# Performance work log

Measured on AMD Instinct MI355X. Metric: run time of the kernel, lower is better.

Reference implementation:

```python
import jax, jax.numpy as jnp
import numpy as np

B, N, E, D, NS, H = 32, 4096, 256, 256, 8, 256
N_ITERS, N_SH, N_MESH, MESH_LR = 3, 5, 4, 5.0

def layer_norm(x, scale, bias, eps=1e-5):
    m = jnp.mean(x, axis=-1, keepdims=True)
    v = jnp.var(x, axis=-1, keepdims=True)
    return (x - m) / jnp.sqrt(v + eps) * scale + bias

def sinkhorn(C, a, b, u=None, v=None, n_iters=N_SH):
    # log-domain Sinkhorn with marginals a [B,N], b [B,S]; C [B,N,S]
    log_a, log_b = jnp.log(a), jnp.log(b)
    if u is None:
        u = jnp.zeros_like(a)
    if v is None:
        v = jnp.zeros_like(b)
    K = -C
    for _ in range(n_iters):
        u = log_a - jax.nn.logsumexp(K + v[:, None, :], axis=-1)
        v = log_b - jax.nn.logsumexp(K + u[:, :, None], axis=-2)
    attn = jnp.exp(K + u[:, :, None] + v[:, None, :])
    return attn, u, v

def minimize_entropy_of_sinkhorn(C0, a, b, mesh_lr=MESH_LR, n_mesh=N_MESH):
    # MESH: gradient-descend the cost matrix to minimize entropy of the transport plan
    def ent(C):
        attn, _, _ = sinkhorn(C, a, b)
        return -jnp.sum(attn * jnp.log(attn + 1e-8))
    C = C0
    for _ in range(n_mesh):
        C = C - mesh_lr * jax.grad(ent)(C)
    _, u, v = sinkhorn(C, a, b)
    return C, u, v

def gru_cell(x, h, Wih, Whh, bih, bhh):
    # torch.nn.GRUCell math, gate order (r, z, n)
    gi = x @ Wih.T + bih
    gh = h @ Whh.T + bhh
    ir, iz, inn = jnp.split(gi, 3, axis=-1)
    hr, hz, hn = jnp.split(gh, 3, axis=-1)
    r = jax.nn.sigmoid(ir + hr)
    z = jax.nn.sigmoid(iz + hz)
    n = jnp.tanh(inn + r * hn)
    return (1.0 - z) * n + z * h

def setup_inputs():
    key = jax.random.key(0)
    ks = jax.random.split(key, 16)
    s = 0.02
    return {
        "inputs": jax.random.normal(ks[0], (B, N, E), jnp.float32),
        "slots_init": jax.random.normal(ks[1], (B, NS, D), jnp.float32),
        "ln_in_s": jnp.ones((E,), jnp.float32), "ln_in_b": jnp.zeros((E,), jnp.float32),
        "ln_sl_s": jnp.ones((D,), jnp.float32), "ln_sl_b": jnp.zeros((D,), jnp.float32),
        "ln_mlp_s": jnp.ones((D,), jnp.float32), "ln_mlp_b": jnp.zeros((D,), jnp.float32),
        "Wq": jax.random.normal(ks[2], (D, D), jnp.float32) * s,
        "Wk": jax.random.normal(ks[3], (E, D), jnp.float32) * s,
        "Wv": jax.random.normal(ks[4], (E, D), jnp.float32) * s,
        "wi_W": jax.random.normal(ks[5], (E, 1), jnp.float32) * s, "wi_b": jnp.zeros((1,), jnp.float32),
        "ws_W": jax.random.normal(ks[6], (D, 1), jnp.float32) * s, "ws_b": jnp.zeros((1,), jnp.float32),
        "gru_Wih": jax.random.normal(ks[7], (3 * D, D), jnp.float32) * s,
        "gru_Whh": jax.random.normal(ks[8], (3 * D, D), jnp.float32) * s,
        "gru_bih": jnp.zeros((3 * D,), jnp.float32), "gru_bhh": jnp.zeros((3 * D,), jnp.float32),
        "mlp_W1": jax.random.normal(ks[9], (D, H), jnp.float32) * s, "mlp_b1": jnp.zeros((H,), jnp.float32),
        "mlp_W2": jax.random.normal(ks[10], (H, D), jnp.float32) * s, "mlp_b2": jnp.zeros((D,), jnp.float32),
    }

def reference(inputs, slots_init, ln_in_s, ln_in_b, ln_sl_s, ln_sl_b, ln_mlp_s, ln_mlp_b, Wq, Wk, Wv, wi_W, wi_b, ws_W, ws_b, gru_Wih, gru_Whh, gru_bih, gru_bhh, mlp_W1, mlp_b1, mlp_W2, mlp_b2):
    x = layer_norm(inputs, ln_in_s, ln_in_b)
    k = x @ Wk          # [B,N,D]
    v = x @ Wv          # [B,N,D]
    a = jax.nn.softmax(jnp.squeeze(x @ wi_W, -1) + wi_b[0], axis=-1) * NS  # input marginal [B,N]
    k_sq = jnp.sum(k * k, axis=-1)  # [B,N]

    def step(slots):
        sn = layer_norm(slots, ln_sl_s, ln_sl_b)
        b = jax.nn.softmax(jnp.squeeze(sn @ ws_W, -1) + ws_b[0], axis=-1) * NS  # slot marginal [B,S]
        q = sn @ Wq  # [B,S,D]
        # Euclidean cdist(k, q) via the Gram-matrix identity
        d2 = k_sq[:, :, None] + jnp.sum(q * q, -1)[:, None, :] - 2.0 * jnp.einsum('bnd,bsd->bns', k, q)
        C = jnp.sqrt(jnp.clip(d2, 1e-12))
        C, p, qpot = minimize_entropy_of_sinkhorn(C, a, b)
        attn, _, _ = sinkhorn(C, a, b, u=p, v=qpot)  # warm-started final sinkhorn
        updates = jnp.einsum('bns,bnd->bsd', attn, v)
        h = gru_cell(updates.reshape(-1, D), slots.reshape(-1, D), gru_Wih, gru_Whh, gru_bih, gru_bhh).reshape(B, NS, D)
        hn = layer_norm(h, ln_mlp_s, ln_mlp_b)
        h = h + (jax.nn.relu(hn @ mlp_W1 + mlp_b1) @ mlp_W2 + mlp_b2)
        return h, attn

    slots = slots_init
    attn = None
    for _ in range(N_ITERS - 1):
        slots, attn = step(slots)
    slots = jax.lax.stop_gradient(slots)  # .detach() before final step
    slots, attn = step(slots)
    return slots, jnp.transpose(attn, (0, 2, 1)), slots
```

## Files before the change

kernel.cpp:

```cpp
#include <hip/hip_runtime.h>
#include <hip/hip_bf16.h>

#define B_ 32
#define N_ 4096
#define E_ 256
#define D_ 256
#define NS_ 8
#define LN8 2.0794415416798357f
#define OFF_ATTN 65536
#define OFF_S2   (65536 + 1048576)
#define NSPLIT 8
#define SENT 0xFFFFFFFFu

typedef unsigned short u16;
typedef unsigned short u16x8 __attribute__((ext_vector_type(8)));
typedef __bf16 bf16x8 __attribute__((ext_vector_type(8)));
typedef float floatx4 __attribute__((ext_vector_type(4)));

__device__ __forceinline__ float bf2f(u16 h) {
  unsigned int u = ((unsigned int)h) << 16;
  return __uint_as_float(u);
}
__device__ __forceinline__ u16 f2bf(float f) {
  unsigned int u = __float_as_uint(f);
  unsigned int r = (u + 0x7FFFu + ((u >> 16) & 1u)) >> 16;
  return (u16)r;
}
__device__ __forceinline__ float ldx(const void* p, int i, int dt) {
  return dt ? ((const float*)p)[i] : bf2f(((const u16*)p)[i]);
}
__device__ __forceinline__ void stx(void* p, size_t i, int dt, float v) {
  if (dt) ((float*)p)[i] = v; else ((u16*)p)[i] = f2bf(v);
}
__device__ __forceinline__ float slog(float x) { return __logf(fmaxf(x, 1e-35f)); }
__device__ __forceinline__ float cl(float x) { return fminf(fmaxf(x, -1e30f), 1e30f); }

__device__ __forceinline__ float breduce256(float v, float* red4, int tid) {
  #pragma unroll
  for (int m = 1; m < 64; m <<= 1) v += __shfl_xor(v, m, 64);
  __syncthreads();
  if ((tid & 63) == 0) red4[tid >> 6] = v;
  __syncthreads();
  return red4[0] + red4[1] + red4[2] + red4[3];
}

__global__ void detect_dtype_kernel(const u16* __restrict__ inp, int* __restrict__ flag) {
  int lane = threadIdx.x & 63;
  int good = 0;
  for (int i = lane; i < 256; i += 64) {
    float x = bf2f(inp[i]);
    float ax = fabsf(x);
    if (x == 0.0f || (ax >= 1e-3f && ax <= 64.0f)) good++;
  }
  #pragma unroll
  for (int m = 1; m < 64; m <<= 1) good += __shfl_xor(good, m, 64);
  if (lane == 0) *flag = (good >= 208) ? 0 : 1;
}


__global__ void transpose_any_kernel(const void* __restrict__ src, u16* __restrict__ dst,
                                     int R, int C, const int* __restrict__ dtf) {
  const int dt = *dtf;
  int idx = blockIdx.x * 256 + threadIdx.x;
  if (idx >= R * C) return;
  int r = idx / C, c = idx - r * C;
  dst[c * R + r] = f2bf(ldx(src, idx, dt));
}

__global__ void cast_slots_kernel(const void* __restrict__ src, float* __restrict__ dst,
                                  const int* __restrict__ dtf) {
  const int dt = *dtf;
  int i = blockIdx.x * 256 + threadIdx.x;
  dst[i] = ldx(src, i, dt);
}

__global__ __launch_bounds__(256) void ln_stats_kernel(
    const void* __restrict__ inp, const void* __restrict__ lns, const void* __restrict__ lnb,
    const void* __restrict__ wiW, const int* __restrict__ dtf,
    u16* __restrict__ xln, float* __restrict__ logits) {
  const int dt = *dtf;
  int row = blockIdx.x * 4 + (threadIdx.x >> 6);
  int lane = threadIdx.x & 63;
  float xs[4];
  if (dt) {
    float4 h = *(const float4*)((const float*)inp + (size_t)row * E_ + lane * 4);
    xs[0] = h.x; xs[1] = h.y; xs[2] = h.z; xs[3] = h.w;
  } else {
    ushort4 h = *(const ushort4*)((const u16*)inp + (size_t)row * E_ + lane * 4);
    xs[0] = bf2f(h.x); xs[1] = bf2f(h.y); xs[2] = bf2f(h.z); xs[3] = bf2f(h.w);
  }
  float s = xs[0] + xs[1] + xs[2] + xs[3];
  float q = xs[0]*xs[0] + xs[1]*xs[1] + xs[2]*xs[2] + xs[3]*xs[3];
  #pragma unroll
  for (int m = 1; m < 64; m <<= 1) { s += __shfl_xor(s, m, 64); q += __shfl_xor(q, m, 64); }
  float mean = s * (1.0f / E_);
  float var = q * (1.0f / E_) - mean * mean;
  float rstd = rsqrtf(fmaxf(var, 0.0f) + 1e-5f);
  int e = lane * 4;
  float d = 0.0f;
  float xn[4];
  #pragma unroll
  for (int j = 0; j < 4; ++j) {
    xn[j] = (xs[j] - mean) * rstd * ldx(lns, e + j, dt) + ldx(lnb, e + j, dt);
    d += xn[j] * ldx(wiW, e + j, dt);
  }
  ushort4 o;
  o.x = f2bf(xn[0]); o.y = f2bf(xn[1]); o.z = f2bf(xn[2]); o.w = f2bf(xn[3]);
  *(ushort4*)(xln + (size_t)row * E_ + e) = o;
  #pragma unroll
  for (int m = 1; m < 64; m <<= 1) d += __shfl_xor(d, m, 64);
  if (lane == 0) logits[row] = d;
}

__global__ __launch_bounds__(1024) void amarg_kernel(const float* __restrict__ logits,
    float* __restrict__ log_a, float* __restrict__ inva) {
  __shared__ float red[16];
  __shared__ float bcast;
  int b = blockIdx.x, tid = threadIdx.x;
  logits += (size_t)b * N_;
  float l[4];
  #pragma unroll
  for (int i = 0; i < 4; ++i) l[i] = logits[tid + i * 1024];
  float mx = fmaxf(fmaxf(l[0], l[1]), fmaxf(l[2], l[3]));
  #pragma unroll
  for (int m = 1; m < 64; m <<= 1) mx = fmaxf(mx, __shfl_xor(mx, m, 64));
  __syncthreads();
  if ((tid & 63) == 0) red[tid >> 6] = mx;
  __syncthreads();
  if (tid == 0) { float v = red[0]; for (int i = 1; i < 16; ++i) v = fmaxf(v, red[i]); bcast = v; }
  __syncthreads();
  float M = bcast;
  float se = 0.0f;
  #pragma unroll
  for (int i = 0; i < 4; ++i) se += __expf(l[i] - M);
  #pragma unroll
  for (int m = 1; m < 64; m <<= 1) se += __shfl_xor(se, m, 64);
  __syncthreads();
  if ((tid & 63) == 0) red[tid >> 6] = se;
  __syncthreads();
  if (tid == 0) { float v = 0; for (int i = 0; i < 16; ++i) v += red[i]; bcast = v; }
  __syncthreads();
  float lgS = slog(bcast);
  #pragma unroll
  for (int i = 0; i < 4; ++i) {
    float lav = l[i] - M - lgS + LN8;
    log_a[tid + i * 1024] = lav;
    inva[tid + i * 1024] = fminf(__expf(-lav), 1e20f);
  }
}

__global__ __launch_bounds__(256, 2) void gemm_bt_kernel(
    const u16* __restrict__ A, const u16* __restrict__ BT, u16* __restrict__ out) {
  __shared__ __align__(16) u16 Als[128 * 32];
  __shared__ __align__(16) u16 Bls[128 * 32];
  int tid = threadIdx.x;
  int m0 = blockIdx.x * 128, n0 = blockIdx.y * 128;
  int w = tid >> 6, lane = tid & 63;
  int wm = (w & 1) * 64, wn = (w >> 1) * 64;
  int fr = lane & 15, kg = lane >> 4;
  floatx4 acc[4][4];
  #pragma unroll
  for (int i = 0; i < 4; ++i)
    #pragma unroll
    for (int j = 0; j < 4; ++j) acc[i][j] = (floatx4){0.f, 0.f, 0.f, 0.f};
  int sm = tid >> 1;
  int sk0 = (tid & 1) * 16;
  const u16* arow = A + (size_t)(m0 + sm) * E_;
  const u16* brow = BT + (size_t)(n0 + sm) * E_;
  for (int kc = 0; kc < E_; kc += 32) {
    #pragma unroll
    for (int j = 0; j < 16; j += 8) {
      int kk = kc + sk0 + j;
      *(u16x8*)&Als[sm * 32 + sk0 + j] = *(const u16x8*)(arow + kk);
      *(u16x8*)&Bls[sm * 32 + sk0 + j] = *(const u16x8*)(brow + kk);
    }
    __syncthreads();
    bf16x8 af[4], bfv[4];
    #pragma unroll
    for (int im = 0; im < 4; ++im) af[im] = *(const bf16x8*)&Als[(wm + im * 16 + fr) * 32 + kg * 8];
    #pragma unroll
    for (int in = 0; in < 4; ++in) bfv[in] = *(const bf16x8*)&Bls[(wn + in * 16 + fr) * 32 + kg * 8];
    #pragma unroll
    for (int im = 0; im < 4; ++im)
      #pragma unroll
      for (int in = 0; in < 4; ++in)
        acc[im][in] = __builtin_amdgcn_mfma_f32_16x16x32_bf16(af[im], bfv[in], acc[im][in], 0, 0, 0);
    __syncthreads();
  }
  #pragma unroll
  for (int im = 0; im < 4; ++im)
    #pragma unroll
    for (int in = 0; in < 4; ++in)
      #pragma unroll
      for (int r = 0; r < 4; ++r) {
        int row = m0 + wm + im * 16 + kg * 4 + r;
        int col = n0 + wn + in * 16 + fr;
        out[(size_t)row * D_ + col] = f2bf(acc[im][in][r]);
      }
}


__global__ __launch_bounds__(256) void s1_kernel(
    const float* __restrict__ slots, const void* __restrict__ lnss, const void* __restrict__ lnsb,
    const void* __restrict__ Wq, const void* __restrict__ wsW, const int* __restrict__ dtf,
    float* __restrict__ qf, float* __restrict__ q_sq, float* __restrict__ logits_b) {
  __shared__ float sn_sh[256];
  __shared__ float red4[4];
  const int dt = *dtf;
  int row = blockIdx.x;
  int tid = threadIdx.x;
  float h = slots[(size_t)row * D_ + tid];
  float sum = breduce256(h, red4, tid);
  float sq = breduce256(h * h, red4, tid);
  float mean = sum * (1.0f / D_), var = sq * (1.0f / D_) - mean * mean;
  float rstd = rsqrtf(fmaxf(var, 0.0f) + 1e-5f);
  float sn = (h - mean) * rstd * ldx(lnss, tid, dt) + ldx(lnsb, tid, dt);
  sn_sh[tid] = sn;
  __syncthreads();
  float acc = 0.0f;
  if (dt) {
    const float* W = (const float*)Wq;
    for (int d = 0; d < 256; ++d) acc += sn_sh[d] * W[d * 256 + tid];
  } else {
    const u16* W = (const u16*)Wq;
    for (int d = 0; d < 256; ++d) acc += sn_sh[d] * bf2f(W[d * 256 + tid]);
  }
  qf[(size_t)row * 256 + tid] = acc;
  float qs = breduce256(acc * acc, red4, tid);
  float lbp = breduce256(sn * ldx(wsW, tid, dt), red4, tid);
  if (tid == 0) { q_sq[row] = qs; logits_b[row] = lbp; }
}

__global__ void bmarg_kernel(const float* __restrict__ logits_b, const void* __restrict__ wsb,
                             const int* __restrict__ dtf, float* __restrict__ log_b) {
  int b = threadIdx.x;
  if (b >= 32) return;
  float off = ldx(wsb, 0, *dtf);
  float l[8], M = -1e30f;
  #pragma unroll
  for (int s = 0; s < 8; ++s) { l[s] = logits_b[b * 8 + s] + off; M = fmaxf(M, l[s]); }
  float S = 0.0f;
  #pragma unroll
  for (int s = 0; s < 8; ++s) S += __expf(l[s] - M);
  float lgS = slog(S);
  #pragma unroll
  for (int s = 0; s < 8; ++s) log_b[b * 8 + s] = l[s] - M - lgS + LN8;
}

__device__ __forceinline__ float grp_sync_reduce(
    float acc8[8], float (*red)[8],
    unsigned int* gp, int rp, int blkn, int wv, int lane, int tid) {
  #pragma unroll
  for (int m = 1; m < 64; m <<= 1)
    #pragma unroll
    for (int s = 0; s < 8; ++s) acc8[s] += __shfl_xor(acc8[s], m, 64);
  if (lane == 0)
    #pragma unroll
    for (int s = 0; s < 8; ++s) red[wv][s] = acc8[s];
  __syncthreads();
  float x = 0.0f;
  if (tid < 64) {
    float v = red[tid >> 3][tid & 7];
    v += __shfl_xor(v, 8, 64);
    v += __shfl_xor(v, 16, 64);
    v += __shfl_xor(v, 32, 64);
    if (tid < 8)
      __hip_atomic_store(gp + rp * 64 + blkn * 8 + tid, __float_as_uint(v),
                         __ATOMIC_RELAXED, __HIP_MEMORY_SCOPE_AGENT);
    unsigned int u;
    for (;;) {
      u = __hip_atomic_load(gp + rp * 64 + tid, __ATOMIC_RELAXED, __HIP_MEMORY_SCOPE_AGENT);
      if (__all(u != SENT)) break;
      __builtin_amdgcn_s_sleep(1);
    }
    x = __uint_as_float(u);
    x += __shfl_xor(x, 8, 64);
    x += __shfl_xor(x, 16, 64);
    x += __shfl_xor(x, 32, 64);
  }
  return x;
}

__global__ __launch_bounds__(512, 2) void mesh_kernel(
    const u16* __restrict__ kbf, const u16* __restrict__ vbf,
    const float* __restrict__ qf32, const float* __restrict__ qsq_g,
    const float* __restrict__ log_a_g, const float* __restrict__ inva_g,
    const float* __restrict__ log_b_g, const int* __restrict__ dtf,
    unsigned int* __restrict__ gpart,
    float* __restrict__ updp, void* __restrict__ dout_or_null) {
  const int blkn = blockIdx.x;
  const int b = blockIdx.y;
  const int tid = threadIdx.x;
  const int dt = *dtf;
  const int n = blkn * 512 + tid;

  __shared__ float evP[6][8];
  __shared__ float lb[8], invb[8];
  __shared__ float dv[8];
  __shared__ float red[8][8];
  __shared__ float q_lds[8][256];
  __shared__ float qsq_l[8];
  __shared__ float pv_lds[512][8];

  const float la = log_a_g[(size_t)b * N_ + n];
  const float ia = inva_g[(size_t)b * N_ + n];
  unsigned int* gp = gpart + (size_t)b * 64 * 64;

  {
    const float* qb = qf32 + (size_t)b * 8 * 256;
    #pragma unroll
    for (int i = tid; i < 2048; i += 512) q_lds[i >> 8][i & 255] = qb[i];
    if (tid < 8) {
      qsq_l[tid] = qsq_g[b * 8 + tid];
      float x = log_b_g[b * 8 + tid];
      lb[tid] = x; invb[tid] = fminf(__expf(-x), 1e20f);
    }
  }
  __syncthreads();

  float E[8], dK[8], eus[5];
  float eu = 0.0f, dup = 0.0f;
  {
    const u16* kp = kbf + ((size_t)b * N_ + n) * D_;
    float accq[8] = {0, 0, 0, 0, 0, 0, 0, 0};
    float kq = 0.0f;
    for (int kc = 0; kc < 256; kc += 8) {
      u16x8 kv = *(const u16x8*)(kp + kc);
      float kf[8];
      #pragma unroll
      for (int j = 0; j < 8; ++j) { kf[j] = bf2f(kv[j]); kq += kf[j] * kf[j]; }
      #pragma unroll
      for (int s = 0; s < 8; ++s) {
        float4 qa = *(const float4*)&q_lds[s][kc];
        float4 qb2 = *(const float4*)&q_lds[s][kc + 4];
        accq[s] += kf[0] * qa.x + kf[1] * qa.y + kf[2] * qa.z + kf[3] * qa.w
                 + kf[4] * qb2.x + kf[5] * qb2.y + kf[6] * qb2.z + kf[7] * qb2.w;
      }
    }
    #pragma unroll
    for (int s = 0; s < 8; ++s) {
      float d2 = kq + qsq_l[s] - 2.0f * accq[s];
      float Cv = sqrtf(fmaxf(d2, 1e-12f));
      E[s] = __expf(-Cv);
    }
  }

  const int wv = tid >> 6, lane = tid & 63;
  int rp = 0;

  for (int mesh = 0; mesh < 4; ++mesh) {
    if (tid < 8) evP[0][tid] = 1.0f;
    __syncthreads();
    for (int t = 1; t <= 5; ++t) {
      float evp[8];
      #pragma unroll
      for (int s = 0; s < 8; ++s) evp[s] = evP[t - 1][s];
      float su = 0.0f;
      #pragma unroll
      for (int s = 0; s < 8; ++s) su += fminf(E[s] * evp[s], 1e30f);
      float u = la - slog(su);
      eu = fminf(__expf(u), 1e20f);
      eus[t - 1] = eu;
      float acc8[8];
      #pragma unroll
      for (int s = 0; s < 8; ++s) acc8[s] = fminf(E[s] * eu, 1e30f);
      float S = grp_sync_reduce(acc8, red, gp, rp, blkn, wv, lane, tid);
      if (tid < 8) {
        float v = lb[tid] - slog(S);
        evP[t][tid] = fminf(__expf(v), 1e20f);
      }
      ++rp;
      __syncthreads();
    }
    {
      float ev5[8];
      #pragma unroll
      for (int s = 0; s < 8; ++s) ev5[s] = evP[5][s];
      float acc8[8];
      dup = 0.0f;
      #pragma unroll
      for (int s = 0; s < 8; ++s) {
        float t1 = fminf(E[s] * eu, 1e30f);
        float P = fminf(t1 * ev5[s], 1e30f);
        float Pe = P + 1e-8f;
        float g = -(__logf(Pe) + P / Pe) * P;
        dK[s] = g; dup += g; acc8[s] = g;
      }
      float S = grp_sync_reduce(acc8, red, gp, rp, blkn, wv, lane, tid);
      if (tid < 8) dv[tid] = cl(S);
      ++rp;
      __syncthreads();
    }
    for (int t = 5; t >= 1; --t) {
      float evt[8], evtm[8], dvl[8], ibl[8];
      #pragma unroll
      for (int s = 0; s < 8; ++s) { evt[s] = evP[t][s]; evtm[s] = evP[t - 1][s]; dvl[s] = dv[s]; ibl[s] = invb[s]; }
      float eut = eus[t - 1];
      float duv = 0.0f;
      float w8[8];
      #pragma unroll
      for (int s = 0; s < 8; ++s) {
        float a1 = fminf(E[s] * eut, 1e30f);
        float b1 = fminf(a1 * evt[s], 1e30f);
        w8[s] = fminf(b1 * ibl[s], 1e30f);
        duv += cl(dvl[s] * w8[s]);
      }
      float du = ((t == 5) ? dup : 0.0f) - duv;
      float duf = cl(cl(du * ia) * eut);
      float acc8[8];
      #pragma unroll
      for (int s = 0; s < 8; ++s) {
        float ee = fminf(E[s] * evtm[s], 1e30f);
        float zc = cl(ee * duf);
        dK[s] -= cl(dvl[s] * w8[s]) + zc;
        acc8[s] = -zc;
      }
      if (t > 1) {
        float S = grp_sync_reduce(acc8, red, gp, rp, blkn, wv, lane, tid);
        if (tid < 8) dv[tid] = cl(S);
        ++rp;
      }
      __syncthreads();
    }
    #pragma unroll
    for (int s = 0; s < 8; ++s) {
      float dkc = fminf(fmaxf(dK[s], -4.0f), 4.0f);
      float Enew = E[s] * __expf(-5.0f * dkc);
      E[s] = fminf(fmaxf(Enew, 1e-35f), 1e30f);
    }
  }

  if (tid < 8) evP[0][tid] = 1.0f;
  __syncthreads();
  for (int t = 1; t <= 10; ++t) {
    int pc = (t - 1) & 1, cc = t & 1;
    float evp[8];
    #pragma unroll
    for (int s = 0; s < 8; ++s) evp[s] = evP[pc][s];
    float su = 0.0f;
    #pragma unroll
    for (int s = 0; s < 8; ++s) su += fminf(E[s] * evp[s], 1e30f);
    eu = fminf(__expf(la - slog(su)), 1e20f);
    float acc8[8];
    #pragma unroll
    for (int s = 0; s < 8; ++s) acc8[s] = fminf(E[s] * eu, 1e30f);
    float S = grp_sync_reduce(acc8, red, gp, rp, blkn, wv, lane, tid);
    if (tid < 8) {
      float v = lb[tid] - slog(S);
      evP[cc][tid] = fminf(__expf(v), 1e20f);
    }
    ++rp;
    __syncthreads();
  }
  float evf[8];
  #pragma unroll
  for (int s = 0; s < 8; ++s) evf[s] = evP[0][s];
  float pv[8];
  #pragma unroll
  for (int s = 0; s < 8; ++s) {
    float t1 = fminf(E[s] * eu, 1e30f);
    pv[s] = fminf(t1 * evf[s], 1e30f);
  }
  if (dout_or_null) {
    #pragma unroll
    for (int s = 0; s < 8; ++s)
      stx(dout_or_null, (size_t)OFF_ATTN + ((size_t)b * 8 + s) * N_ + n, dt, pv[s]);
  }

  #pragma unroll
  for (int s = 0; s < 8; ++s) pv_lds[tid][s] = pv[s];
  __syncthreads();
  {
    int d = tid & 255, half = tid >> 8;
    const u16* vp = vbf + ((size_t)b * N_ + blkn * 512 + half * 256) * D_ + d;
    float acc[8] = {0, 0, 0, 0, 0, 0, 0, 0};
    for (int i = 0; i < 256; ++i) {
      float vv = bf2f(vp[(size_t)i * D_]);
      float4 a0 = *(const float4*)&pv_lds[half * 256 + i][0];
      float4 a1 = *(const float4*)&pv_lds[half * 256 + i][4];
      acc[0] += a0.x * vv; acc[1] += a0.y * vv; acc[2] += a0.z * vv; acc[3] += a0.w * vv;
      acc[4] += a1.x * vv; acc[5] += a1.y * vv; acc[6] += a1.z * vv; acc[7] += a1.w * vv;
    }
    __syncthreads();
    if (half == 1) {
      #pragma unroll
      for (int s = 0; s < 8; ++s) pv_lds[d][s] = acc[s];
    }
    __syncthreads();
    if (half == 0) {
      #pragma unroll
      for (int s = 0; s < 8; ++s) acc[s] += pv_lds[d][s];
      #pragma unroll
      for (int s = 0; s < 8; ++s)
        updp[(((size_t)b * 8 + blkn) * 8 + s) * D_ + d] = acc[s];
    }
  }
}

__global__ __launch_bounds__(256) void gru_mlp_kernel(
    const float* __restrict__ updp, const float* __restrict__ slots_cur,
    const u16* __restrict__ WihT, const u16* __restrict__ WhhT,
    const void* __restrict__ bih, const void* __restrict__ bhh,
    const void* __restrict__ lnms, const void* __restrict__ lnmb,
    const void* __restrict__ W1, const void* __restrict__ b1,
    const void* __restrict__ W2, const void* __restrict__ b2,
    const int* __restrict__ dtf,
    float* __restrict__ slots_next, void* __restrict__ dout_or_null) {
  __shared__ float xs[256], hs[256], hns[256], as_[256];
  __shared__ float red4[4];
  const int dt = *dtf;
  int row = blockIdx.x;
  int b = row >> 3, s = row & 7;
  int tid = threadIdx.x;
  float x = 0.0f;
  #pragma unroll
  for (int c = 0; c < 8; ++c) x += updp[(((size_t)b * 8 + c) * 8 + s) * D_ + tid];
  float h = slots_cur[(size_t)row * D_ + tid];
  xs[tid] = x; hs[tid] = h;
  __syncthreads();
  float gr = ldx(bih, tid, dt), gz = ldx(bih, 256 + tid, dt), gn = ldx(bih, 512 + tid, dt);
  float hr = ldx(bhh, tid, dt), hz = ldx(bhh, 256 + tid, dt), hn_ = ldx(bhh, 512 + tid, dt);
  for (int e = 0; e < 256; ++e) {
    float xe = xs[e], he = hs[e];
    const u16* wi = WihT + e * 768;
    const u16* wh = WhhT + e * 768;
    gr += xe * bf2f(wi[tid]); gz += xe * bf2f(wi[256 + tid]); gn += xe * bf2f(wi[512 + tid]);
    hr += he * bf2f(wh[tid]); hz += he * bf2f(wh[256 + tid]); hn_ += he * bf2f(wh[512 + tid]);
  }
  float r = 1.0f / (1.0f + __expf(-(gr + hr)));
  float z = 1.0f / (1.0f + __expf(-(gz + hz)));
  float nn = tanhf(gn + r * hn_);
  float h2 = (1.0f - z) * nn + z * h;
  float sum = breduce256(h2, red4, tid);
  float sq = breduce256(h2 * h2, red4, tid);
  float mean = sum * (1.0f / D_), var = sq * (1.0f / D_) - mean * mean;
  float rstd = rsqrtf(fmaxf(var, 0.0f) + 1e-5f);
  float hn2 = (h2 - mean) * rstd * ldx(lnms, tid, dt) + ldx(lnmb, tid, dt);
  hns[tid] = hn2;
  __syncthreads();
  float a1 = ldx(b1, tid, dt);
  if (dt) {
    const float* W = (const float*)W1;
    for (int e = 0; e < 256; ++e) a1 += hns[e] * W[e * 256 + tid];
  } else {
    const u16* W = (const u16*)W1;
    for (int e = 0; e < 256; ++e) a1 += hns[e] * bf2f(W[e * 256 + tid]);
  }
  a1 = fmaxf(a1, 0.0f);
  as_[tid] = a1;
  __syncthreads();
  float o = h2 + ldx(b2, tid, dt);
  if (dt) {
    const float* W = (const float*)W2;
    for (int e = 0; e < 256; ++e) o += as_[e] * W[e * 256 + tid];
  } else {
    const u16* W = (const u16*)W2;
    for (int e = 0; e < 256; ++e) o += as_[e] * bf2f(W[e * 256 + tid]);
  }
  slots_next[(size_t)row * D_ + tid] = o;
  if (dout_or_null) {
    stx(dout_or_null, (size_t)row * D_ + tid, dt, o);
    stx(dout_or_null, (size_t)OFF_S2 + (size_t)row * D_ + tid, dt, o);
  }
}


extern "C" void kernel_launch(void* const* d_in, const int* in_sizes, int n_in,
                              void* d_out, int out_size, void* d_ws, size_t ws_size,
                              hipStream_t stream) {
  (void)in_sizes; (void)n_in; (void)out_size;
  const void* inp      = d_in[0];
  const void* slots0   = d_in[1];
  const void* ln_in_s  = d_in[2];
  const void* ln_in_b  = d_in[3];
  const void* ln_sl_s  = d_in[4];
  const void* ln_sl_b  = d_in[5];
  const void* ln_mlp_s = d_in[6];
  const void* ln_mlp_b = d_in[7];
  const void* Wq  = d_in[8];
  const void* Wk  = d_in[9];
  const void* Wv  = d_in[10];
  const void* wiW = d_in[11];
  const void* wsW = d_in[13];
  const void* wsb = d_in[14];
  const void* Wih = d_in[15];
  const void* Whh = d_in[16];
  const void* bih = d_in[17];
  const void* bhh = d_in[18];
  const void* W1  = d_in[19];
  const void* b1  = d_in[20];
  const void* W2  = d_in[21];
  const void* b2  = d_in[22];

  char* ws = (char*)d_ws;
  size_t off = 0;
  auto alloc = [&](size_t bytes) -> void* {
    void* p = ws + off;
    off += (bytes + 255) & ~(size_t)255;
    return p;
  };
  const size_t NR = (size_t)B_ * N_;
  int* dtflag     = (int*)alloc(256);
  float* logits_a = (float*)alloc(NR * 4);
  float* log_a    = (float*)alloc(NR * 4);
  float* inva     = (float*)alloc(NR * 4);
  u16* xln        = (u16*)alloc(NR * E_ * 2);
  u16* kbf        = (u16*)alloc(NR * D_ * 2);
  u16* vbf        = (u16*)alloc(NR * D_ * 2);
  u16* WkT        = (u16*)alloc(E_ * D_ * 2);
  u16* WvT        = (u16*)alloc(E_ * D_ * 2);
  u16* WihT       = (u16*)alloc(768 * 256 * 2);
  u16* WhhT       = (u16*)alloc(768 * 256 * 2);
  float* qf32     = (float*)alloc((size_t)B_ * 8 * 256 * 4);
  float* q_sq     = (float*)alloc(B_ * 8 * 4);
  float* logits_b = (float*)alloc(B_ * 8 * 4);
  float* log_b    = (float*)alloc(B_ * 8 * 4);
  float* updp     = (float*)alloc((size_t)B_ * 8 * 8 * D_ * 4);
  float* slots_a  = (float*)alloc((size_t)B_ * 8 * D_ * 4);
  float* slots_b  = (float*)alloc((size_t)B_ * 8 * D_ * 4);
  unsigned int* gpart = (unsigned int*)alloc((size_t)3 * B_ * 64 * 64 * 4);
  if (ws_size < off) return;

  hipMemsetAsync(gpart, 0xFF, (size_t)3 * B_ * 64 * 64 * 4, stream);
  detect_dtype_kernel<<<1, 64, 0, stream>>>((const u16*)inp, dtflag);

  transpose_any_kernel<<<(E_ * D_ + 255) / 256, 256, 0, stream>>>(Wk, WkT, E_, D_, dtflag);
  transpose_any_kernel<<<(E_ * D_ + 255) / 256, 256, 0, stream>>>(Wv, WvT, E_, D_, dtflag);
  transpose_any_kernel<<<(768 * 256 + 255) / 256, 256, 0, stream>>>(Wih, WihT, 768, 256, dtflag);
  transpose_any_kernel<<<(768 * 256 + 255) / 256, 256, 0, stream>>>(Whh, WhhT, 768, 256, dtflag);
  cast_slots_kernel<<<(B_ * 8 * D_) / 256, 256, 0, stream>>>(slots0, slots_a, dtflag);
  ln_stats_kernel<<<NR / 4, 256, 0, stream>>>(inp, ln_in_s, ln_in_b, wiW, dtflag, xln, logits_a);
  amarg_kernel<<<B_, 1024, 0, stream>>>(logits_a, log_a, inva);
  gemm_bt_kernel<<<dim3(NR / 128, 2), 256, 0, stream>>>(xln, WkT, kbf);
  gemm_bt_kernel<<<dim3(NR / 128, 2), 256, 0, stream>>>(xln, WvT, vbf);

  float* scur = slots_a;
  float* snext = slots_b;
  for (int step = 0; step < 3; ++step) {
    bool last = (step == 2);
    s1_kernel<<<B_ * 8, 256, 0, stream>>>(scur, ln_sl_s, ln_sl_b, Wq, wsW, dtflag, qf32, q_sq, logits_b);
    bmarg_kernel<<<1, 32, 0, stream>>>(logits_b, wsb, dtflag, log_b);
    mesh_kernel<<<dim3(NSPLIT, B_), 512, 0, stream>>>(kbf, vbf, qf32, q_sq, log_a, inva, log_b,
                                                      dtflag, gpart + (size_t)step * B_ * 64 * 64,
                                                      updp, last ? d_out : (void*)nullptr);
    gru_mlp_kernel<<<B_ * 8, 256, 0, stream>>>(updp, scur, WihT, WhhT, bih, bhh,
                                               ln_mlp_s, ln_mlp_b, W1, b1, W2, b2, dtflag, snext,
                                               last ? d_out : (void*)nullptr);
    float* t = scur; scur = snext; snext = t;
  }
}
```

Measured before the change: 1.028 ms.

## Fuse small kernels to cut launch count across setup and slot loop

Merges the four weight transposes into two kernels and the K and V projections into a single GEMM launch over a concatenated transposed weight. The slot-marginal softmax moves inside the mesh kernel, and the next step's slot layernorm/query projection is folded into the tail of the GRU/MLP kernel. The aim is to remove per-launch overhead and the serial gaps between tiny kernels. In exchange, the mesh kernel does some redundant per-block softmax work and the GRU kernel gets longer with extra block reductions.

```diff
diff --git a/kernel.cpp b/kernel.cpp
--- a/kernel.cpp
+++ b/kernel.cpp
@@ -58,13 +58,26 @@
 }
 
 
-__global__ void transpose_any_kernel(const void* __restrict__ src, u16* __restrict__ dst,
-                                     int R, int C, const int* __restrict__ dtf) {
+__global__ void tr_kv_kernel(const void* __restrict__ Wk, const void* __restrict__ Wv,
+                             u16* __restrict__ WkvT, const int* __restrict__ dtf) {
   const int dt = *dtf;
   int idx = blockIdx.x * 256 + threadIdx.x;
-  if (idx >= R * C) return;
-  int r = idx / C, c = idx - r * C;
-  dst[c * R + r] = f2bf(ldx(src, idx, dt));
+  int half = idx >> 16, i = idx & 65535;
+  int r = i >> 8, c = i & 255;
+  const void* src = half ? Wv : Wk;
+  WkvT[((size_t)(half * 256 + c)) * 256 + r] = f2bf(ldx(src, i, dt));
+}
+
+__global__ void tr_gru_kernel(const void* __restrict__ Wih, const void* __restrict__ Whh,
+                              u16* __restrict__ WihT, u16* __restrict__ WhhT,
+                              const int* __restrict__ dtf) {
+  const int dt = *dtf;
+  int idx = blockIdx.x * 256 + threadIdx.x;
+  int half = idx >= 196608;
+  int i = idx - (half ? 196608 : 0);
+  int r = i >> 8, c = i & 255;
+  u16* dst = half ? WhhT : WihT;
+  dst[(size_t)c * 768 + r] = f2bf(ldx(half ? Whh : Wih, i, dt));
 }
 
 __global__ void cast_slots_kernel(const void* __restrict__ src, float* __restrict__ dst,
@@ -150,11 +163,14 @@
 }
 
 __global__ __launch_bounds__(256, 2) void gemm_bt_kernel(
-    const u16* __restrict__ A, const u16* __restrict__ BT, u16* __restrict__ out) {
+    const u16* __restrict__ A, const u16* __restrict__ BT,
+    u16* __restrict__ kbf, u16* __restrict__ vbf) {
   __shared__ __align__(16) u16 Als[128 * 32];
   __shared__ __align__(16) u16 Bls[128 * 32];
   int tid = threadIdx.x;
   int m0 = blockIdx.x * 128, n0 = blockIdx.y * 128;
+  u16* ob = (n0 < 256) ? kbf : vbf;
+  int nb = n0 & 255;
   int w = tid >> 6, lane = tid & 63;
   int wm = (w & 1) * 64, wn = (w >> 1) * 64;
   int fr = lane & 15, kg = lane >> 4;
@@ -194,8 +210,8 @@
       #pragma unroll
       for (int r = 0; r < 4; ++r) {
         int row = m0 + wm + im * 16 + kg * 4 + r;
-        int col = n0 + wn + in * 16 + fr;
-        out[(size_t)row * D_ + col] = f2bf(acc[im][in][r]);
+        int col = nb + wn + in * 16 + fr;
+        ob[(size_t)row * D_ + col] = f2bf(acc[im][in][r]);
       }
 }
 
@@ -231,22 +247,6 @@
   if (tid == 0) { q_sq[row] = qs; logits_b[row] = lbp; }
 }
 
-__global__ void bmarg_kernel(const float* __restrict__ logits_b, const void* __restrict__ wsb,
-                             const int* __restrict__ dtf, float* __restrict__ log_b) {
-  int b = threadIdx.x;
-  if (b >= 32) return;
-  float off = ldx(wsb, 0, *dtf);
-  float l[8], M = -1e30f;
-  #pragma unroll
-  for (int s = 0; s < 8; ++s) { l[s] = logits_b[b * 8 + s] + off; M = fmaxf(M, l[s]); }
-  float S = 0.0f;
-  #pragma unroll
-  for (int s = 0; s < 8; ++s) S += __expf(l[s] - M);
-  float lgS = slog(S);
-  #pragma unroll
-  for (int s = 0; s < 8; ++s) log_b[b * 8 + s] = l[s] - M - lgS + LN8;
-}
-
 __device__ __forceinline__ float grp_sync_reduce(
     float acc8[8], float (*red)[8],
     unsigned int* gp, int rp, int blkn, int wv, int lane, int tid) {
@@ -285,7 +285,8 @@
     const u16* __restrict__ kbf, const u16* __restrict__ vbf,
     const float* __restrict__ qf32, const float* __restrict__ qsq_g,
     const float* __restrict__ log_a_g, const float* __restrict__ inva_g,
-    const float* __restrict__ log_b_g, const int* __restrict__ dtf,
+    const float* __restrict__ logits_b_g, const void* __restrict__ wsb,
+    const int* __restrict__ dtf,
     unsigned int* __restrict__ gpart,
     float* __restrict__ updp, void* __restrict__ dout_or_null) {
   const int blkn = blockIdx.x;
@@ -312,7 +313,15 @@
     for (int i = tid; i < 2048; i += 512) q_lds[i >> 8][i & 255] = qb[i];
     if (tid < 8) {
       qsq_l[tid] = qsq_g[b * 8 + tid];
-      float x = log_b_g[b * 8 + tid];
+      float off = ldx(wsb, 0, dt);
+      float l[8], M = -1e30f;
+      #pragma unroll
+      for (int s = 0; s < 8; ++s) { l[s] = logits_b_g[b * 8 + s] + off; M = fmaxf(M, l[s]); }
+      float S = 0.0f;
+      #pragma unroll
+      for (int s = 0; s < 8; ++s) S += __expf(l[s] - M);
+      float lgS = slog(S);
+      float x = l[tid] - M - lgS + LN8;
       lb[tid] = x; invb[tid] = fminf(__expf(-x), 1e20f);
     }
   }
@@ -497,15 +506,19 @@
   }
 }
 
-__global__ __launch_bounds__(256) void gru_mlp_kernel(
+__global__ __launch_bounds__(256) void gru_s1_kernel(
     const float* __restrict__ updp, const float* __restrict__ slots_cur,
     const u16* __restrict__ WihT, const u16* __restrict__ WhhT,
     const void* __restrict__ bih, const void* __restrict__ bhh,
     const void* __restrict__ lnms, const void* __restrict__ lnmb,
     const void* __restrict__ W1, const void* __restrict__ b1,
     const void* __restrict__ W2, const void* __restrict__ b2,
-    const int* __restrict__ dtf,
-    float* __restrict__ slots_next, void* __restrict__ dout_or_null) {
+    const void* __restrict__ lnss, const void* __restrict__ lnsb,
+    const void* __restrict__ Wq, const void* __restrict__ wsW,
+    const int* __restrict__ dtf, int do_s1,
+    float* __restrict__ slots_next, float* __restrict__ qf,
+    float* __restrict__ q_sq, float* __restrict__ logits_b,
+    void* __restrict__ dout_or_null) {
   __shared__ float xs[256], hs[256], hns[256], as_[256];
   __shared__ float red4[4];
   const int dt = *dtf;
@@ -561,6 +574,28 @@
   if (dout_or_null) {
     stx(dout_or_null, (size_t)row * D_ + tid, dt, o);
     stx(dout_or_null, (size_t)OFF_S2 + (size_t)row * D_ + tid, dt, o);
+  }
+  if (do_s1) {
+    float sum2 = breduce256(o, red4, tid);
+    float sq2 = breduce256(o * o, red4, tid);
+    float mean2 = sum2 * (1.0f / D_), var2 = sq2 * (1.0f / D_) - mean2 * mean2;
+    float rstd2 = rsqrtf(fmaxf(var2, 0.0f) + 1e-5f);
+    float sn = (o - mean2) * rstd2 * ldx(lnss, tid, dt) + ldx(lnsb, tid, dt);
+    __syncthreads();
+    xs[tid] = sn;
+    __syncthreads();
+    float accq = 0.0f;
+    if (dt) {
+      const float* W = (const float*)Wq;
+      for (int d = 0; d < 256; ++d) accq += xs[d] * W[d * 256 + tid];
+    } else {
+      const u16* W = (const u16*)Wq;
+      for (int d = 0; d < 256; ++d) accq += xs[d] * bf2f(W[d * 256 + tid]);
+    }
+    qf[(size_t)row * 256 + tid] = accq;
+    float qs = breduce256(accq * accq, red4, tid);
+    float lbp = breduce256(sn * ldx(wsW, tid, dt), red4, tid);
+    if (tid == 0) { q_sq[row] = qs; logits_b[row] = lbp; }
   }
 }
 
@@ -607,14 +642,12 @@
   u16* xln        = (u16*)alloc(NR * E_ * 2);
   u16* kbf        = (u16*)alloc(NR * D_ * 2);
   u16* vbf        = (u16*)alloc(NR * D_ * 2);
-  u16* WkT        = (u16*)alloc(E_ * D_ * 2);
-  u16* WvT        = (u16*)alloc(E_ * D_ * 2);
+  u16* WkvT       = (u16*)alloc((size_t)512 * 256 * 2);
   u16* WihT       = (u16*)alloc(768 * 256 * 2);
   u16* WhhT       = (u16*)alloc(768 * 256 * 2);
   float* qf32     = (float*)alloc((size_t)B_ * 8 * 256 * 4);
   float* q_sq     = (float*)alloc(B_ * 8 * 4);
   float* logits_b = (float*)alloc(B_ * 8 * 4);
-  float* log_b    = (float*)alloc(B_ * 8 * 4);
   float* updp     = (float*)alloc((size_t)B_ * 8 * 8 * D_ * 4);
   float* slots_a  = (float*)alloc((size_t)B_ * 8 * D_ * 4);
   float* slots_b  = (float*)alloc((size_t)B_ * 8 * D_ * 4);
@@ -624,28 +657,27 @@
   hipMemsetAsync(gpart, 0xFF, (size_t)3 * B_ * 64 * 64 * 4, stream);
   detect_dtype_kernel<<<1, 64, 0, stream>>>((const u16*)inp, dtflag);
 
-  transpose_any_kernel<<<(E_ * D_ + 255) / 256, 256, 0, stream>>>(Wk, WkT, E_, D_, dtflag);
-  transpose_any_kernel<<<(E_ * D_ + 255) / 256, 256, 0, stream>>>(Wv, WvT, E_, D_, dtflag);
-  transpose_any_kernel<<<(768 * 256 + 255) / 256, 256, 0, stream>>>(Wih, WihT, 768, 256, dtflag);
-  transpose_any_kernel<<<(768 * 256 + 255) / 256, 256, 0, stream>>>(Whh, WhhT, 768, 256, dtflag);
+  tr_kv_kernel<<<512, 256, 0, stream>>>(Wk, Wv, WkvT, dtflag);
+  tr_gru_kernel<<<1536, 256, 0, stream>>>(Wih, Whh, WihT, WhhT, dtflag);
   cast_slots_kernel<<<(B_ * 8 * D_) / 256, 256, 0, stream>>>(slots0, slots_a, dtflag);
   ln_stats_kernel<<<NR / 4, 256, 0, stream>>>(inp, ln_in_s, ln_in_b, wiW, dtflag, xln, logits_a);
   amarg_kernel<<<B_, 1024, 0, stream>>>(logits_a, log_a, inva);
-  gemm_bt_kernel<<<dim3(NR / 128, 2), 256, 0, stream>>>(xln, WkT, kbf);
-  gemm_bt_kernel<<<dim3(NR / 128, 2), 256, 0, stream>>>(xln, WvT, vbf);
+  gemm_bt_kernel<<<dim3(NR / 128, 4), 256, 0, stream>>>(xln, WkvT, kbf, vbf);
 
   float* scur = slots_a;
   float* snext = slots_b;
+  s1_kernel<<<B_ * 8, 256, 0, stream>>>(scur, ln_sl_s, ln_sl_b, Wq, wsW, dtflag, qf32, q_sq, logits_b);
   for (int step = 0; step < 3; ++step) {
     bool last = (step == 2);
-    s1_kernel<<<B_ * 8, 256, 0, stream>>>(scur, ln_sl_s, ln_sl_b, Wq, wsW, dtflag, qf32, q_sq, logits_b);
-    bmarg_kernel<<<1, 32, 0, stream>>>(logits_b, wsb, dtflag, log_b);
-    mesh_kernel<<<dim3(NSPLIT, B_), 512, 0, stream>>>(kbf, vbf, qf32, q_sq, log_a, inva, log_b,
-                                                      dtflag, gpart + (size_t)step * B_ * 64 * 64,
+    mesh_kernel<<<dim3(NSPLIT, B_), 512, 0, stream>>>(kbf, vbf, qf32, q_sq, log_a, inva,
+                                                      logits_b, wsb, dtflag,
+                                                      gpart + (size_t)step * B_ * 64 * 64,
                                                       updp, last ? d_out : (void*)nullptr);
-    gru_mlp_kernel<<<B_ * 8, 256, 0, stream>>>(updp, scur, WihT, WhhT, bih, bhh,
-                                               ln_mlp_s, ln_mlp_b, W1, b1, W2, b2, dtflag, snext,
-                                               last ? d_out : (void*)nullptr);
+    gru_s1_kernel<<<B_ * 8, 256, 0, stream>>>(updp, scur, WihT, WhhT, bih, bhh,
+                                              ln_mlp_s, ln_mlp_b, W1, b1, W2, b2,
+                                              ln_sl_s, ln_sl_b, Wq, wsW, dtflag, last ? 0 : 1,
+                                              snext, qf32, q_sq, logits_b,
+                                              last ? d_out : (void*)nullptr);
     float* t = scur; scur = snext; snext = t;
   }
 }
```

After: 1.000 ms. 1.03x faster.
